# Performance work log

Hardware: AMD Instinct MI355X
Metric: run time of the kernel (lower is better)

Reference implementation:

```python
import jax, jax.numpy as jnp
import numpy as np

K = 3  # Chebyshev order (number of coefficients)


def setup_inputs() -> dict:
    key = jax.random.key(0)
    k1, k2, k3, k4 = jax.random.split(key, 4)
    B, nNode, c_in, T = 16, 512, 32, 64
    c_out = 64
    x = jax.random.normal(k1, (B, nNode, c_in, T), dtype=jnp.float32)
    # scaled Laplacian-like batched adjacency; scale keeps the Chebyshev
    # recursion numerically tame (spectral norm ~ O(1))
    adj = jax.random.normal(k2, (B, nNode, nNode), dtype=jnp.float32) * (1.0 / np.sqrt(nNode))
    # 1x1 conv params: weight [c_out, K*c_in], bias [c_out]
    W = jax.random.normal(k3, (c_out, K * c_in), dtype=jnp.float32) * 0.1
    b = jax.random.normal(k4, (c_out,), dtype=jnp.float32) * 0.1
    return {"x": x, "adj": adj, "W": W, "b": b}


def reference(x, adj, W, b):
    # x: [B, nNode, c_in, T] -> permute(0,2,1,3) -> [B, c_in, nNode, T]
    x = jnp.transpose(x, (0, 2, 1, 3))
    B, c_in, nNode, T = x.shape
    # Chebyshev recursion: L0 = I, L1 = adj, L_k = 2*adj@L_{k-1} - L_{k-2}
    L0 = jnp.broadcast_to(jnp.eye(nNode, dtype=x.dtype), (B, nNode, nNode))
    L1 = adj
    Ls = [L0, L1]
    for _ in range(2, K):
        L2 = 2.0 * jnp.matmul(adj, L1) - L0
        L0, L1 = L1, L2
        Ls.append(L2)
    Lap = jnp.stack(Ls, axis=1)              # [B, K, nNode, nNode]
    Lap = jnp.swapaxes(Lap, -1, -2)          # transpose(-1, -2)
    # einsum 'bcnl,bknq->bckql' then view [B, c_in*K, nNode, T]
    y = jnp.einsum('bcnl,bknq->bckql', x, Lap)  # [B, c_in, K, nNode, T]
    y = y.reshape(B, c_in * K, nNode, T)
    # 1x1 Conv2d: channel mixing + bias
    out = jnp.einsum('oc,bcnl->bonl', W, y) + b[None, :, None, None]
    return out
```

## Files before the change

kernel.cpp:

```cpp
#include <hip/hip_runtime.h>

typedef unsigned short u16;
typedef __bf16 v8bf __attribute__((ext_vector_type(8)));
typedef float f32x4 __attribute__((ext_vector_type(4)));
typedef u16 us8 __attribute__((ext_vector_type(8)));
typedef u16 us4 __attribute__((ext_vector_type(4)));

static __device__ __forceinline__ u16 f2bf(float f) {
  union { __bf16 h; u16 u; } cv;
  cv.h = (__bf16)f;
  return cv.u;
}

static __device__ __forceinline__ void gl_lds16(const u16* g, u16* l) {
  __builtin_amdgcn_global_load_lds(
      (const __attribute__((address_space(1))) unsigned int*)g,
      (__attribute__((address_space(3))) unsigned int*)l, 16, 0, 0);
}

__global__ __launch_bounds__(256)
void prep_k(const float* __restrict__ adj, u16* __restrict__ adjC,
            u16* __restrict__ adjT_bf, const float* __restrict__ x,
            u16* __restrict__ xT, u16* __restrict__ SV,
            const float* __restrict__ W, u16* __restrict__ Mb) {
  const int bid = blockIdx.x;
  const int tid = threadIdx.x;
  __shared__ u16 Ls[64][68];
  if (bid < 1024) {
    const int b = bid >> 6;
    const int r0 = ((bid >> 3) & 7) * 64;
    const int c0 = (bid & 7) * 64;
#pragma unroll
    for (int i = 0; i < 4; ++i) {
      const int idx = tid + 256 * i;
      const int r = idx >> 4;
      const int c4 = (idx & 15) * 4;
      const float4 v = *(const float4*)(adj + ((size_t)(b * 512 + r0 + r) * 512 + c0 + c4));
      us4 o;
      o[0] = f2bf(v.x); o[1] = f2bf(v.y); o[2] = f2bf(v.z); o[3] = f2bf(v.w);
      *(us4*)&Ls[r][c4] = o;
      *(us4*)(adjC + ((size_t)(b * 1024 + r0 + r) * 512 + c0 + c4)) = o;
    }
    __syncthreads();
#pragma unroll
    for (int i = 0; i < 2; ++i) {
      const int idx = tid + 256 * i;
      const int c = idx >> 3;
      const int r8 = (idx & 7) * 8;
      us8 o;
#pragma unroll
      for (int j = 0; j < 8; ++j) o[j] = Ls[r8 + j][c];
      *(us8*)(adjT_bf + ((size_t)(b * 512 + c0 + c) * 512 + r0 + r8)) = o;
    }
  } else if (bid < 5120) {
    const int t = bid - 1024;
    const int b = t >> 8;
    const int q0 = ((t >> 5) & 7) * 64;
    const int j0 = (t & 31) * 64;
#pragma unroll
    for (int i = 0; i < 4; ++i) {
      const int idx = tid + 256 * i;
      const int r = idx >> 4;
      const int j4 = (idx & 15) * 4;
      const float4 v = *(const float4*)(x + ((size_t)(b * 512 + q0 + r) * 2048 + j0 + j4));
      us4 o;
      o[0] = f2bf(v.x); o[1] = f2bf(v.y); o[2] = f2bf(v.z); o[3] = f2bf(v.w);
      *(us4*)&Ls[r][j4] = o;
      *(us4*)(SV + ((size_t)(b * 1536 + q0 + r) * 2048 + j0 + j4)) = o;
    }
    __syncthreads();
#pragma unroll
    for (int i = 0; i < 2; ++i) {
      const int idx = tid + 256 * i;
      const int jp = idx >> 3;
      const int q8 = (idx & 7) * 8;
      us8 o;
#pragma unroll
      for (int j = 0; j < 8; ++j) o[j] = Ls[q8 + j][jp];
      *(us8*)(xT + ((size_t)(b * 2048 + j0 + jp) * 512 + q0 + q8)) = o;
    }
  } else {
    for (int i = tid; i < 64 * 96; i += 256) {
      const int cc = i % 96;
      const int r = cc % 3;
      const float w = W[i];
      const float m = (r == 0) ? (w - W[i + 2]) : w;
      Mb[i] = f2bf(m);
    }
  }
}

__global__ __launch_bounds__(256)
void gemm_sq(const u16* __restrict__ adjC_in, const u16* __restrict__ BT,
             u16* __restrict__ adjC) {
  const int b = blockIdx.z;
  const int row0 = blockIdx.y * 128;
  const int col0 = blockIdx.x * 128;
  const u16* Ab = adjC_in + (size_t)b * 1024 * 512;
  const u16* BTb = BT + (size_t)b * 512 * 512;

  __shared__ u16 smem[16384];
  u16* As = smem;
  u16* Bs = smem + 8192;

  const int tid = threadIdx.x;
  const int lane = tid & 63;
  const int w = tid >> 6;
  const int wm = (w >> 1) * 64;
  const int wn = (w & 1) * 64;
  const int l16 = lane & 15;
  const int kg = lane >> 4;

  f32x4 acc[4][4];
#pragma unroll
  for (int m = 0; m < 4; ++m)
#pragma unroll
    for (int n = 0; n < 4; ++n) acc[m][n] = (f32x4){0.f, 0.f, 0.f, 0.f};

  for (int k0 = 0; k0 < 512; k0 += 64) {
    __syncthreads();
#pragma unroll
    for (int i = 0; i < 4; ++i) {
      const int eb = w * 2048 + i * 512;
      const int e = eb + lane * 8;
      const int r = e >> 6;
      const int kk = e & 63;
      gl_lds16(Ab + (size_t)(row0 + r) * 512 + k0 + kk, As + eb);
      gl_lds16(BTb + (size_t)(col0 + r) * 512 + k0 + kk, Bs + eb);
    }
    __syncthreads();
#pragma unroll
    for (int ks = 0; ks < 2; ++ks) {
      v8bf af[4], bfr[4];
#pragma unroll
      for (int m = 0; m < 4; ++m)
        af[m] = *(const v8bf*)(As + (wm + m * 16 + l16) * 64 + ks * 32 + kg * 8);
#pragma unroll
      for (int n = 0; n < 4; ++n)
        bfr[n] = *(const v8bf*)(Bs + (wn + n * 16 + l16) * 64 + ks * 32 + kg * 8);
#pragma unroll
      for (int m = 0; m < 4; ++m)
#pragma unroll
        for (int n = 0; n < 4; ++n)
          acc[m][n] = __builtin_amdgcn_mfma_f32_16x16x32_bf16(af[m], bfr[n], acc[m][n], 0, 0, 0);
    }
  }
  u16* Cb = adjC + (size_t)b * 1024 * 512 + (size_t)512 * 512;
#pragma unroll
  for (int m = 0; m < 4; ++m)
#pragma unroll
    for (int n = 0; n < 4; ++n)
#pragma unroll
      for (int v = 0; v < 4; ++v) {
        const int rr = row0 + wm + m * 16 + kg * 4 + v;
        const int cc = col0 + wn + n * 16 + l16;
        Cb[(size_t)rr * 512 + cc] = f2bf(2.0f * acc[m][n][v]);
      }
}

__global__ __launch_bounds__(256)
void prop_k(const u16* __restrict__ AC, const u16* __restrict__ BT,
            u16* __restrict__ SV) {
  const int fid = blockIdx.x + 16 * (blockIdx.y + 8 * blockIdx.z);
  const int wk = (fid & 7) * 256 + (fid >> 3);
  const int b = wk >> 7;
  const int row0 = ((wk >> 4) & 7) * 128;
  const int col0 = (wk & 15) * 128;
  const u16* Ab = AC + (size_t)b * 1024 * 512;
  const u16* BTb = BT + (size_t)b * 2048 * 512;

  __shared__ u16 smem[16384];
  u16* As = smem;
  u16* Bs = smem + 8192;

  const int tid = threadIdx.x;
  const int lane = tid & 63;
  const int w = tid >> 6;
  const int wm = (w >> 1) * 64;
  const int wn = (w & 1) * 64;
  const int l16 = lane & 15;
  const int kg = lane >> 4;

  f32x4 acc[4][4];
#pragma unroll
  for (int m = 0; m < 4; ++m)
#pragma unroll
    for (int n = 0; n < 4; ++n) acc[m][n] = (f32x4){0.f, 0.f, 0.f, 0.f};

  for (int k0 = 0; k0 < 512; k0 += 64) {
    __syncthreads();
#pragma unroll
    for (int i = 0; i < 4; ++i) {
      const int eb = w * 2048 + i * 512;
      const int e = eb + lane * 8;
      const int r = e >> 6;
      const int kk = e & 63;
      gl_lds16(Ab + (size_t)(row0 + r) * 512 + k0 + kk, As + eb);
      gl_lds16(BTb + (size_t)(col0 + r) * 512 + k0 + kk, Bs + eb);
    }
    __syncthreads();
#pragma unroll
    for (int ks = 0; ks < 2; ++ks) {
      v8bf af[4], bfr[4];
#pragma unroll
      for (int m = 0; m < 4; ++m)
        af[m] = *(const v8bf*)(As + (wm + m * 16 + l16) * 64 + ks * 32 + kg * 8);
#pragma unroll
      for (int n = 0; n < 4; ++n)
        bfr[n] = *(const v8bf*)(Bs + (wn + n * 16 + l16) * 64 + ks * 32 + kg * 8);
#pragma unroll
      for (int m = 0; m < 4; ++m)
#pragma unroll
        for (int n = 0; n < 4; ++n)
          acc[m][n] = __builtin_amdgcn_mfma_f32_16x16x32_bf16(af[m], bfr[n], acc[m][n], 0, 0, 0);
    }
  }
  u16* Cb = SV + (size_t)b * 1536 * 2048 + (size_t)512 * 2048;
#pragma unroll
  for (int m = 0; m < 4; ++m)
#pragma unroll
    for (int n = 0; n < 4; ++n)
#pragma unroll
      for (int v = 0; v < 4; ++v) {
        const int rr = row0 + wm + m * 16 + kg * 4 + v;
        const int cc = col0 + wn + n * 16 + l16;
        Cb[(size_t)rr * 2048 + cc] = f2bf(acc[m][n][v]);
      }
}

__global__ __launch_bounds__(256)
void mix_mfma(const u16* __restrict__ SV, const u16* __restrict__ Mb,
              const float* __restrict__ bias, float* __restrict__ out) {
  const int q = blockIdx.x;
  const int b = blockIdx.y;
  __shared__ u16 Vt[64][104];
  __shared__ u16 Ms[64][104];
  const int tid = threadIdx.x;
  const int lane = tid & 63;
  const int w = tid >> 6;
  const int l16 = lane & 15;
  const int kg = lane >> 4;

#pragma unroll
  for (int i = 0; i < 3; ++i) {
    const int idx = tid + 256 * i;
    const int o = idx / 12;
    const int c8 = (idx % 12) * 8;
    *(uint4*)&Ms[o][c8] = *(const uint4*)(Mb + o * 96 + c8);
  }
  const size_t base = ((size_t)b * 1536 + q) * 2048;
  {
    const int c = tid >> 3;
    const int l0 = (tid & 7) * 8;
    const us8 v0 = *(const us8*)(SV + base + c * 64 + l0);
    const us8 v1 = *(const us8*)(SV + base + (size_t)512 * 2048 + c * 64 + l0);
    const us8 v2 = *(const us8*)(SV + base + (size_t)1024 * 2048 + c * 64 + l0);
#pragma unroll
    for (int j = 0; j < 8; ++j) {
      Vt[l0 + j][3 * c + 0] = v0[j];
      Vt[l0 + j][3 * c + 1] = v1[j];
      Vt[l0 + j][3 * c + 2] = v2[j];
    }
  }
  __syncthreads();

  f32x4 acc[4];
#pragma unroll
  for (int n = 0; n < 4; ++n) acc[n] = (f32x4){0.f, 0.f, 0.f, 0.f};
#pragma unroll
  for (int ks = 0; ks < 3; ++ks) {
    const v8bf a = *(const v8bf*)&Ms[w * 16 + l16][ks * 32 + kg * 8];
#pragma unroll
    for (int n = 0; n < 4; ++n) {
      const v8bf bv = *(const v8bf*)&Vt[n * 16 + l16][ks * 32 + kg * 8];
      acc[n] = __builtin_amdgcn_mfma_f32_16x16x32_bf16(a, bv, acc[n], 0, 0, 0);
    }
  }
#pragma unroll
  for (int n = 0; n < 4; ++n)
#pragma unroll
    for (int v = 0; v < 4; ++v) {
      const int o = w * 16 + kg * 4 + v;
      out[(((size_t)b * 64 + o) * 512 + q) * 64 + n * 16 + l16] = acc[n][v] + bias[o];
    }
}

extern "C" void kernel_launch(void* const* d_in, const int* in_sizes, int n_in,
                              void* d_out, int out_size, void* d_ws, size_t ws_size,
                              hipStream_t stream) {
  const float* x   = (const float*)d_in[0];
  const float* adj = (const float*)d_in[1];
  const float* W   = (const float*)d_in[2];
  const float* bia = (const float*)d_in[3];
  float* out = (float*)d_out;

  u16* adjC    = (u16*)d_ws;
  u16* adjT_bf = adjC    + (size_t)16 * 1024 * 512;
  u16* xT      = adjT_bf + (size_t)16 * 512 * 512;
  u16* SV      = xT      + (size_t)16 * 2048 * 512;
  u16* Mb      = SV      + (size_t)16 * 1536 * 2048;

  hipLaunchKernelGGL(prep_k, dim3(5121), dim3(256), 0, stream,
                     adj, adjC, adjT_bf, x, xT, SV, W, Mb);
  hipLaunchKernelGGL(gemm_sq, dim3(4, 4, 16), dim3(256), 0, stream,
                     adjC, adjT_bf, adjC);
  hipLaunchKernelGGL(prop_k, dim3(16, 8, 16), dim3(256), 0, stream,
                     adjC, xT, SV);
  hipLaunchKernelGGL(mix_mfma, dim3(512, 16), dim3(256), 0, stream,
                     SV, Mb, bia, out);
}
```

Before: 160.1 us.

## Enlarge prop_k tile to 256x128 with 512 threads and 32x32x16 MFMA

Reworks the propagation GEMM so each block covers a 256x128 output tile with 8 waves instead of 128x128 with 4, halving the grid. It also switches from 16x16x32 to 32x32x16 bf16 MFMA, giving each wave a 64x64 tile held as 2x2 32x32 accumulators. The goal is better reuse of the B operand per block and fewer LDS fragment loads per MFMA. In exchange it uses more LDS per block, launches fewer blocks (1024), and may reduce occupancy.

```diff
diff --git a/kernel.cpp b/kernel.cpp
--- a/kernel.cpp
+++ b/kernel.cpp
@@ -3,6 +3,7 @@
 typedef unsigned short u16;
 typedef __bf16 v8bf __attribute__((ext_vector_type(8)));
 typedef float f32x4 __attribute__((ext_vector_type(4)));
+typedef float f32x16 __attribute__((ext_vector_type(16)));
 typedef u16 us8 __attribute__((ext_vector_type(8)));
 typedef u16 us4 __attribute__((ext_vector_type(4)));
 
@@ -158,73 +159,79 @@
       }
 }
 
-__global__ __launch_bounds__(256)
+__global__ __launch_bounds__(512)
 void prop_k(const u16* __restrict__ AC, const u16* __restrict__ BT,
             u16* __restrict__ SV) {
-  const int fid = blockIdx.x + 16 * (blockIdx.y + 8 * blockIdx.z);
-  const int wk = (fid & 7) * 256 + (fid >> 3);
-  const int b = wk >> 7;
-  const int row0 = ((wk >> 4) & 7) * 128;
+  const int fid = blockIdx.x + 16 * (blockIdx.y + 4 * blockIdx.z);
+  const int wk = (fid & 7) * 128 + (fid >> 3);
+  const int b = wk >> 6;
+  const int row0 = ((wk >> 4) & 3) * 256;
   const int col0 = (wk & 15) * 128;
   const u16* Ab = AC + (size_t)b * 1024 * 512;
   const u16* BTb = BT + (size_t)b * 2048 * 512;
 
-  __shared__ u16 smem[16384];
+  __shared__ u16 smem[24576];
   u16* As = smem;
-  u16* Bs = smem + 8192;
+  u16* Bs = smem + 16384;
 
   const int tid = threadIdx.x;
   const int lane = tid & 63;
   const int w = tid >> 6;
   const int wm = (w >> 1) * 64;
   const int wn = (w & 1) * 64;
-  const int l16 = lane & 15;
-  const int kg = lane >> 4;
-
-  f32x4 acc[4][4];
-#pragma unroll
-  for (int m = 0; m < 4; ++m)
-#pragma unroll
-    for (int n = 0; n < 4; ++n) acc[m][n] = (f32x4){0.f, 0.f, 0.f, 0.f};
+  const int l32 = lane & 31;
+  const int hk = lane >> 5;
+
+  f32x16 acc[2][2];
+#pragma unroll
+  for (int mi = 0; mi < 2; ++mi)
+#pragma unroll
+    for (int ni = 0; ni < 2; ++ni)
+#pragma unroll
+      for (int v = 0; v < 16; ++v) acc[mi][ni][v] = 0.f;
 
   for (int k0 = 0; k0 < 512; k0 += 64) {
     __syncthreads();
 #pragma unroll
     for (int i = 0; i < 4; ++i) {
-      const int eb = w * 2048 + i * 512;
-      const int e = eb + lane * 8;
-      const int r = e >> 6;
-      const int kk = e & 63;
-      gl_lds16(Ab + (size_t)(row0 + r) * 512 + k0 + kk, As + eb);
-      gl_lds16(BTb + (size_t)(col0 + r) * 512 + k0 + kk, Bs + eb);
-    }
-    __syncthreads();
-#pragma unroll
-    for (int ks = 0; ks < 2; ++ks) {
-      v8bf af[4], bfr[4];
-#pragma unroll
-      for (int m = 0; m < 4; ++m)
-        af[m] = *(const v8bf*)(As + (wm + m * 16 + l16) * 64 + ks * 32 + kg * 8);
-#pragma unroll
-      for (int n = 0; n < 4; ++n)
-        bfr[n] = *(const v8bf*)(Bs + (wn + n * 16 + l16) * 64 + ks * 32 + kg * 8);
-#pragma unroll
-      for (int m = 0; m < 4; ++m)
-#pragma unroll
-        for (int n = 0; n < 4; ++n)
-          acc[m][n] = __builtin_amdgcn_mfma_f32_16x16x32_bf16(af[m], bfr[n], acc[m][n], 0, 0, 0);
-    }
-  }
+      const int cb = w * 64 + i * 512;
+      const int e = (cb + lane) * 8;
+      gl_lds16(Ab + (size_t)(row0 + (e >> 6)) * 512 + k0 + (e & 63), As + cb * 8);
+    }
+#pragma unroll
+    for (int i = 0; i < 2; ++i) {
+      const int cb = w * 64 + i * 512;
+      const int e = (cb + lane) * 8;
+      gl_lds16(BTb + (size_t)(col0 + (e >> 6)) * 512 + k0 + (e & 63), Bs + cb * 8);
+    }
+    __syncthreads();
+#pragma unroll
+    for (int ks = 0; ks < 4; ++ks) {
+      v8bf af[2], bf[2];
+#pragma unroll
+      for (int mi = 0; mi < 2; ++mi)
+        af[mi] = *(const v8bf*)(As + (wm + mi * 32 + l32) * 64 + ks * 16 + hk * 8);
+#pragma unroll
+      for (int ni = 0; ni < 2; ++ni)
+        bf[ni] = *(const v8bf*)(Bs + (wn + ni * 32 + l32) * 64 + ks * 16 + hk * 8);
+#pragma unroll
+      for (int mi = 0; mi < 2; ++mi)
+#pragma unroll
+        for (int ni = 0; ni < 2; ++ni)
+          acc[mi][ni] = __builtin_amdgcn_mfma_f32_32x32x16_bf16(af[mi], bf[ni], acc[mi][ni], 0, 0, 0);
+    }
+  }
+
   u16* Cb = SV + (size_t)b * 1536 * 2048 + (size_t)512 * 2048;
 #pragma unroll
-  for (int m = 0; m < 4; ++m)
-#pragma unroll
-    for (int n = 0; n < 4; ++n)
-#pragma unroll
-      for (int v = 0; v < 4; ++v) {
-        const int rr = row0 + wm + m * 16 + kg * 4 + v;
-        const int cc = col0 + wn + n * 16 + l16;
-        Cb[(size_t)rr * 2048 + cc] = f2bf(acc[m][n][v]);
+  for (int mi = 0; mi < 2; ++mi)
+#pragma unroll
+    for (int ni = 0; ni < 2; ++ni)
+#pragma unroll
+      for (int r = 0; r < 16; ++r) {
+        const int rr = row0 + wm + mi * 32 + (r & 3) + 8 * (r >> 2) + 4 * hk;
+        const int cc = col0 + wn + ni * 32 + l32;
+        Cb[(size_t)rr * 2048 + cc] = f2bf(acc[mi][ni][r]);
       }
 }
 
@@ -304,7 +311,7 @@
                      adj, adjC, adjT_bf, x, xT, SV, W, Mb);
   hipLaunchKernelGGL(gemm_sq, dim3(4, 4, 16), dim3(256), 0, stream,
                      adjC, adjT_bf, adjC);
-  hipLaunchKernelGGL(prop_k, dim3(16, 8, 16), dim3(256), 0, stream,
+  hipLaunchKernelGGL(prop_k, dim3(16, 4, 16), dim3(512), 0, stream,
                      adjC, xT, SV);
   hipLaunchKernelGGL(mix_mfma, dim3(512, 16), dim3(256), 0, stream,
                      SV, Mb, bia, out);
```

New measurement: 173.9 us. +8.6%, slower.
